# Optimization experiments

Measured on AMD Instinct MI355X. Metric: run time of the kernel, lower is better.

Reference implementation:

```python
import jax, jax.numpy as jnp
import numpy as np

N = 50000          # nodes
E = 800000         # edges
F_IN = 64          # node_features (== LSTM hidden)
C = 100            # conv_out_channels of GatedGraphConv
T = 8              # n_target


def setup_inputs() -> dict:
    key = jax.random.key(0)
    ks = jax.random.split(key, 20)
    s = 0.05
    return {
        "x": jax.random.normal(ks[0], (N, F_IN), jnp.float32),
        "edge_index": jax.random.randint(ks[1], (2, E), 0, N, jnp.int64),
        "edge_weight": jax.random.uniform(ks[2], (E,), jnp.float32),
        "h_0": jax.random.normal(ks[3], (1, N, F_IN), jnp.float32),
        "c_0": jax.random.normal(ks[4], (1, N, F_IN), jnp.float32),
        # GatedGraphConv: weight [num_layers=1, C, C]
        "ggc_w": jax.random.normal(ks[5], (1, C, C), jnp.float32) * s,
        # GRUCell(C, C)
        "gru_w_ih": jax.random.normal(ks[6], (3 * C, C), jnp.float32) * s,
        "gru_w_hh": jax.random.normal(ks[7], (3 * C, C), jnp.float32) * s,
        "gru_b_ih": jnp.zeros((3 * C,), jnp.float32),
        "gru_b_hh": jnp.zeros((3 * C,), jnp.float32),
        # LSTM(input=C, hidden=F_IN, num_layers=1)
        "lstm_w_ih": jax.random.normal(ks[8], (4 * F_IN, C), jnp.float32) * s,
        "lstm_w_hh": jax.random.normal(ks[9], (4 * F_IN, F_IN), jnp.float32) * s,
        "lstm_b_ih": jnp.zeros((4 * F_IN,), jnp.float32),
        "lstm_b_hh": jnp.zeros((4 * F_IN,), jnp.float32),
        # final Linear(F_IN -> T)
        "lin_w": jax.random.normal(ks[10], (T, F_IN), jnp.float32) * s,
        "lin_b": jnp.zeros((T,), jnp.float32),
    }


def reference(x, edge_index, edge_weight, h_0, c_0,
              ggc_w, gru_w_ih, gru_w_hh, gru_b_ih, gru_b_hh,
              lstm_w_ih, lstm_w_hh, lstm_b_ih, lstm_b_hh, lin_w, lin_b):
    src, dst = edge_index[0], edge_index[1]
    # --- GatedGraphConv (1 layer, mean aggr) ---
    xp = jnp.pad(x, ((0, 0), (0, C - x.shape[1])))  # pad features to C
    m = xp @ ggc_w[0]                               # [N, C]
    msg = m[src] * edge_weight[:, None]             # [E, C] gather + weight
    summ = jax.ops.segment_sum(msg, dst, num_segments=N)
    cnt = jax.ops.segment_sum(jnp.ones_like(edge_weight), dst, num_segments=N)
    agg = summ / jnp.maximum(cnt, 1.0)[:, None]     # scatter-mean
    # GRUCell(agg, xp)
    gi = agg @ gru_w_ih.T + gru_b_ih
    gh = xp @ gru_w_hh.T + gru_b_hh
    i_r, i_z, i_n = jnp.split(gi, 3, axis=1)
    h_r, h_z, h_n = jnp.split(gh, 3, axis=1)
    r = jax.nn.sigmoid(i_r + h_r)
    z = jax.nn.sigmoid(i_z + h_z)
    n = jnp.tanh(i_n + r * h_n)
    conv_h = (1.0 - z) * n + z * xp                 # [N, C]
    # --- LSTM, one time step, batch=N, hidden=F_IN ---
    gates = conv_h @ lstm_w_ih.T + lstm_b_ih + h_0[0] @ lstm_w_hh.T + lstm_b_hh
    i_g, f_g, g_g, o_g = jnp.split(gates, 4, axis=1)
    i_g = jax.nn.sigmoid(i_g)
    f_g = jax.nn.sigmoid(f_g)
    g_g = jnp.tanh(g_g)
    o_g = jax.nn.sigmoid(o_g)
    c1 = f_g * c_0[0] + i_g * g_g                   # [N, F_IN]
    h1 = o_g * jnp.tanh(c1)                         # [N, F_IN]
    # --- relu + linear head ---
    out = jax.nn.relu(h1) @ lin_w.T + lin_b         # [N, T]
    return out, h1[None], c1[None]
```

## Files before the change

### kernel.cpp

```cpp
#include <hip/hip_runtime.h>

#define N_NODES 50000
#define N_EDGES 800000
#define F_INF   64
#define C_CH    100
#define T_OUT   8

typedef unsigned short u16;
typedef unsigned int   u32;
typedef __attribute__((ext_vector_type(8))) short bf16x8;
typedef __attribute__((ext_vector_type(4))) float f32x4;

__device__ __forceinline__ float sigmoidf_(float x) {
    return 1.0f / (1.0f + __expf(-x));
}
__device__ __forceinline__ float tanhf_(float x) {
    return 1.0f - 2.0f / (__expf(2.0f * x) + 1.0f);
}
__device__ __forceinline__ u16 f2bf(float f) {
    union { float f; u32 u; } v; v.f = f;
    u32 u = v.u;
    u += 0x7FFF + ((u >> 16) & 1);
    return (u16)(u >> 16);
}
__device__ __forceinline__ float bf2f(u16 h) {
    union { u32 u; float f; } v; v.u = ((u32)h) << 16;
    return v.f;
}
__device__ __forceinline__ float asf_(int i) {
    union { int i; float f; } v; v.i = i; return v.f;
}

#define BK_NPB 64
#define BK_NB  ((N_NODES + BK_NPB - 1) / BK_NPB)
#define BCAP   1280
#define PART_T     1024
#define PART_CHUNK 8192
#define PART_B ((N_EDGES + PART_CHUNK - 1) / PART_CHUNK)
#define PP_XBF_B 391
#define WG2_ELEMS (7 * 4 * 4 * 64 * 8)
#define WL2_ELEMS (4 * 6 * 4 * 64 * 8)
#define PP_W_B ((WG2_ELEMS + WL2_ELEMS) / 1024)
#define PP_B (PART_B + PP_XBF_B + PP_W_B)
#define PP_LDS_SIZE 110880
__global__ __launch_bounds__(PART_T) void k_pp(
    const int* __restrict__ ei, const float* __restrict__ ew,
    const float* __restrict__ x,
    const float* __restrict__ ggc, const float* __restrict__ gwih,
    const float* __restrict__ gwhh,
    const float* __restrict__ lwih, const float* __restrict__ lwhh,
    int* __restrict__ bcur, int2* __restrict__ bucket,
    u16* __restrict__ xbf, u16* __restrict__ Wg2, u16* __restrict__ Wl2) {
    extern __shared__ __align__(16) char pls[];
    int gb = blockIdx.x;
    int tid = threadIdx.x;

    if (gb < PART_B) {
        int2* se    = (int2*)pls;
        int*  gdst  = (int*)(pls + 65536);
        int*  hist  = (int*)(pls + 98304);
        int*  ebase = (int*)(pls + 101432);
        int*  cur   = (int*)(pls + 104560);
        int*  gbase = (int*)(pls + 107688);
        int*  wsum  = (int*)(pls + 110816);
        int e0 = gb * PART_CHUNK;
        int cnt = N_EDGES - e0;
        if (cnt > PART_CHUNK) cnt = PART_CHUNK;

        for (int i = tid; i < BK_NB; i += PART_T) hist[i] = 0;
        __syncthreads();

        int srcr[8], dstr[8]; float wvr[8];
#pragma unroll
        for (int k = 0; k < 8; ++k) {
            int e = tid + k * PART_T;
            if (e < cnt) {
                srcr[k] = ei[e0 + e];
                dstr[k] = ei[N_EDGES + e0 + e];
                wvr[k]  = ew[e0 + e];
                atomicAdd(&hist[dstr[k] >> 6], 1);
            } else dstr[k] = -1;
        }
        __syncthreads();

        {
            int lane = tid & 63, w = tid >> 6;
            int h = (tid < BK_NB) ? hist[tid] : 0;
            int v = h;
#pragma unroll
            for (int off = 1; off < 64; off <<= 1) {
                int u = __shfl_up(v, off, 64);
                if (lane >= off) v += u;
            }
            if (lane == 63) wsum[w] = v;
            __syncthreads();
            if (tid < 16) {
                int s = wsum[tid];
#pragma unroll
                for (int off = 1; off < 16; off <<= 1) {
                    int u = __shfl_up(s, off, 16);
                    if (tid >= off) s += u;
                }
                wsum[tid] = s;
            }
            __syncthreads();
            if (tid < BK_NB) {
                int v2 = v + ((w > 0) ? wsum[w - 1] : 0);
                int ex = v2 - h;
                ebase[tid] = ex;
                cur[tid] = ex;
                gbase[tid] = (h > 0) ? atomicAdd(&bcur[tid * 16], h) : 0;
            }
        }
        __syncthreads();

#pragma unroll
        for (int k = 0; k < 8; ++k) {
            if (dstr[k] >= 0) {
                int b = dstr[k] >> 6;
                int p = atomicAdd(&cur[b], 1);
                int gl = gbase[b] + (p - ebase[b]);
                se[p] = make_int2(srcr[k] | ((dstr[k] & 63) << 16), __float_as_int(wvr[k]));
                gdst[p] = (gl < BCAP) ? (b * BCAP + gl) : -1;
            }
        }
        __syncthreads();

        for (int i = tid; i < cnt; i += PART_T) {
            int g = gdst[i];
            if (g >= 0) bucket[g] = se[i];
        }
        return;
    }

    if (gb < PART_B + PP_XBF_B) {
        int idx = (gb - PART_B) * 1024 + tid;
        if (idx >= N_NODES * F_INF / 8) return;
        float4 a = ((const float4*)x)[idx * 2];
        float4 b = ((const float4*)x)[idx * 2 + 1];
        uint4 p;
        p.x = (u32)f2bf(a.x) | ((u32)f2bf(a.y) << 16);
        p.y = (u32)f2bf(a.z) | ((u32)f2bf(a.w) << 16);
        p.z = (u32)f2bf(b.x) | ((u32)f2bf(b.y) << 16);
        p.w = (u32)f2bf(b.z) | ((u32)f2bf(b.w) << 16);
        ((uint4*)xbf)[idx] = p;
        return;
    }

    int idx = (gb - PART_B - PP_XBF_B) * 1024 + tid;
    if (idx < WG2_ELEMS) {
        int e    = idx & 7;
        int lane = (idx >> 3) & 63;
        int g    = (idx >> 9) & 3;
        int kt   = (idx >> 11) & 3;
        int ct   = idx >> 13;
        int c = ct * 16 + (lane & 15);
        int k = kt * 32 + (lane >> 4) * 8 + e;
        float val = 0.0f;
        if (c < 100) {
            if (g < 3) {
                if (k < 64) {
                    const float* wr = gwih + (g * 100 + c) * 100;
                    const float* gr = ggc + k * 100;
                    float s = 0.0f;
#pragma unroll 4
                    for (int j = 0; j < 100; ++j) s += wr[j] * gr[j];
                    val = s;
                } else if (g < 2) {
                    val = gwhh[(g * 100 + c) * 100 + (k - 64)];
                }
            } else {
                if (k >= 64) val = gwhh[(200 + c) * 100 + (k - 64)];
            }
        }
        Wg2[idx] = f2bf(val);
    } else if (idx < WG2_ELEMS + WL2_ELEMS) {
        int i2 = idx - WG2_ELEMS;
        int e    = i2 & 7;
        int lane = (i2 >> 3) & 63;
        int g    = (i2 >> 9) & 3;
        int ctkt = i2 >> 11;
        int ct = ctkt / 6, kt = ctkt - ct * 6;
        int c = ct * 16 + (lane & 15);
        int k = kt * 32 + (lane >> 4) * 8 + e;
        float val = 0.0f;
        if (k < 100) val = lwih[(g * 64 + c) * 100 + k];
        else if (k >= 128) val = lwhh[(g * 64 + c) * 64 + (k - 128)];
        Wl2[i2] = f2bf(val);
    }
}

__global__ __launch_bounds__(512, 3) void k_bagg(
    const int2* __restrict__ bucket, const int* __restrict__ bcur,
    const u16* __restrict__ xbf, u16* __restrict__ xaggbf) {
    __shared__ int2 se[BCAP];
    __shared__ int  hist[64];
    __shared__ int  base[65];
    __shared__ int  cur[64];
    int tid = threadIdx.x;
    int b = blockIdx.x;
    int n0 = b * BK_NPB;

    if (tid < 64) hist[tid] = 0;
    __syncthreads();

    int cnt = bcur[b * 16];
    if (cnt > BCAP) cnt = BCAP;
    const int2* mybkt = bucket + (size_t)b * BCAP;

    int2 r0 = make_int2(0, 0), r1 = make_int2(0, 0), r2 = make_int2(0, 0);
    int nr = 0;
    if (tid < cnt)        { r0 = mybkt[tid];        atomicAdd(&hist[(r0.x >> 16) & 63], 1); nr = 1; }
    if (tid + 512 < cnt)  { r1 = mybkt[tid + 512];  atomicAdd(&hist[(r1.x >> 16) & 63], 1); nr = 2; }
    if (tid + 1024 < cnt) { r2 = mybkt[tid + 1024]; atomicAdd(&hist[(r2.x >> 16) & 63], 1); nr = 3; }
    __syncthreads();

    if (tid < 64) {
        int h = hist[tid];
        int v = h;
#pragma unroll
        for (int off = 1; off < 64; off <<= 1) {
            int u = __shfl_up(v, off, 64);
            if (tid >= off) v += u;
        }
        base[tid + 1] = v;
        if (tid == 0) base[0] = 0;
        cur[tid] = v - h;
    }
    __syncthreads();

    if (nr > 0) { int p = atomicAdd(&cur[(r0.x >> 16) & 63], 1); se[p] = r0; }
    if (nr > 1) { int p = atomicAdd(&cur[(r1.x >> 16) & 63], 1); se[p] = r1; }
    if (nr > 2) { int p = atomicAdd(&cur[(r2.x >> 16) & 63], 1); se[p] = r2; }
    __syncthreads();

    int w = tid >> 6, lane = tid & 63;
#pragma unroll
    for (int j = 0; j < 8; ++j) {
        int nl = w * 8 + j;
        int s = base[nl], epos = base[nl + 1];
        float acc = 0.0f;
        int i = s;
        for (; i + 3 < epos; i += 4) {
            int2 e0 = se[i], e1 = se[i + 1], e2 = se[i + 2], e3 = se[i + 3];
            float v0 = bf2f(xbf[(size_t)(e0.x & 0xFFFF) * 64 + lane]);
            float v1 = bf2f(xbf[(size_t)(e1.x & 0xFFFF) * 64 + lane]);
            float v2 = bf2f(xbf[(size_t)(e2.x & 0xFFFF) * 64 + lane]);
            float v3 = bf2f(xbf[(size_t)(e3.x & 0xFFFF) * 64 + lane]);
            acc += v0 * asf_(e0.y); acc += v1 * asf_(e1.y);
            acc += v2 * asf_(e2.y); acc += v3 * asf_(e3.y);
        }
        for (; i < epos; ++i) {
            int2 e0 = se[i];
            acc += bf2f(xbf[(size_t)(e0.x & 0xFFFF) * 64 + lane]) * asf_(e0.y);
        }
        int n = n0 + nl;
        if (n < N_NODES) {
            acc /= fmaxf((float)(epos - s), 1.0f);
            xaggbf[(size_t)n * 64 + lane] = f2bf(acc);
        }
    }
}

#define RNN_A2   9728
#define RNN_BIAS 23552
#define RNN_BL   25952
#define RNN_LWF  26976
#define RNN_LBS  29024
__global__ __launch_bounds__(256, 4) void k_rnn(
    const u16* __restrict__ xaggbf, const u16* __restrict__ xbf,
    const float* __restrict__ h0, const float* __restrict__ c0,
    const u16* __restrict__ Wg2, const u16* __restrict__ Wl2,
    const float* __restrict__ gbih, const float* __restrict__ gbhh,
    const float* __restrict__ lbih, const float* __restrict__ lbhh,
    const float* __restrict__ lw, const float* __restrict__ lb,
    float* __restrict__ out, float* __restrict__ h1, float* __restrict__ c1) {
    __shared__ __align__(16) char smem[29056];
    u16*   A1   = (u16*)(smem);
    u16*   A2   = (u16*)(smem + RNN_A2);
    float* bias = (float*)(smem + RNN_BIAS);
    float* bl   = (float*)(smem + RNN_BL);
    float* lwf  = (float*)(smem + RNN_LWF);
    float* lbs  = (float*)(smem + RNN_LBS);
    float* h1s  = (float*)(smem);
    int tid = threadIdx.x;
    int n0 = blockIdx.x * 32;
    int w = tid >> 6, lane = tid & 63, quad = lane >> 4, ln = lane & 15;

    float c0r[2][4];
    {
        int c = w * 16 + ln;
#pragma unroll
        for (int mt = 0; mt < 2; ++mt)
#pragma unroll
            for (int reg = 0; reg < 4; ++reg) {
                int n = n0 + mt * 16 + quad * 4 + reg;
                c0r[mt][reg] = (n < N_NODES) ? c0[(size_t)n * F_INF + c] : 0.0f;
            }
    }
    for (int i = tid; i < 512; i += 256) {
        int row = i >> 4, ch = i & 15;
        int n = n0 + row;
        uint4 v = make_uint4(0, 0, 0, 0);
        if (n < N_NODES)
            v = (ch < 8) ? ((const uint4*)xaggbf)[n * 8 + ch]
                         : ((const uint4*)xbf)[n * 8 + (ch - 8)];
        *(uint4*)(A1 + row * 152 + ch * 8) = v;
    }
    {
        int row = tid >> 3, ch = tid & 7;
        int n = n0 + row;
        uint4 p = make_uint4(0, 0, 0, 0);
        if (n < N_NODES) {
            float4 f0 = ((const float4*)h0)[n * 16 + ch * 2];
            float4 f1 = ((const float4*)h0)[n * 16 + ch * 2 + 1];
            p.x = (u32)f2bf(f0.x) | ((u32)f2bf(f0.y) << 16);
            p.y = (u32)f2bf(f0.z) | ((u32)f2bf(f0.w) << 16);
            p.z = (u32)f2bf(f1.x) | ((u32)f2bf(f1.y) << 16);
            p.w = (u32)f2bf(f1.z) | ((u32)f2bf(f1.w) << 16);
        }
        *(uint4*)(A2 + row * 216 + 128 + ch * 8) = p;
    }
    if (tid < 64) {
        int row = tid >> 1, ch2 = tid & 1;
        *(uint4*)(A2 + row * 216 + 112 + ch2 * 8) = make_uint4(0, 0, 0, 0);
    }
    for (int i = tid; i < 600; i += 256)
        bias[i] = (i < 300) ? gbih[i] : gbhh[i - 300];
    if (tid < 256) bl[tid] = lbih[tid] + lbhh[tid];
    for (int i = tid; i < 512; i += 256) {
        int k = i >> 3, t = i & 7;
        lwf[i] = lw[t * F_INF + k];
    }
    if (tid < 8) lbs[tid] = lb[tid];
    __syncthreads();

    for (int ct = w; ct < 7; ct += 4) {
        int c = ct * 16 + ln;
        float br = 0.f, bz = 0.f, bn2 = 0.f, bh2 = 0.f;
        if (c < 100) {
            br  = bias[c]       + bias[300 + c];
            bz  = bias[100 + c] + bias[400 + c];
            bn2 = bias[200 + c];
            bh2 = bias[500 + c];
        }
        f32x4 ar[2], az[2], an[2], ah[2];
#pragma unroll
        for (int mt = 0; mt < 2; ++mt) {
            ar[mt] = (f32x4){0.f, 0.f, 0.f, 0.f};
            az[mt] = ar[mt]; an[mt] = ar[mt]; ah[mt] = ar[mt];
        }
        const bf16x8* wp = (const bf16x8*)Wg2 + (size_t)(ct * 16) * 64 + lane;
#pragma unroll
        for (int kt = 0; kt < 4; ++kt) {
            bf16x8 b0 = wp[(kt * 4 + 0) * 64];
            bf16x8 b1 = wp[(kt * 4 + 1) * 64];
            bf16x8 b2 = wp[(kt * 4 + 2) * 64];
            bf16x8 b3 = wp[(kt * 4 + 3) * 64];
#pragma unroll
            for (int mt = 0; mt < 2; ++mt) {
                bf16x8 a = *(const bf16x8*)(A1 + (mt * 16 + ln) * 152 + kt * 32 + quad * 8);
                ar[mt] = __builtin_amdgcn_mfma_f32_16x16x32_bf16(a, b0, ar[mt], 0, 0, 0);
                az[mt] = __builtin_amdgcn_mfma_f32_16x16x32_bf16(a, b1, az[mt], 0, 0, 0);
                an[mt] = __builtin_amdgcn_mfma_f32_16x16x32_bf16(a, b2, an[mt], 0, 0, 0);
                ah[mt] = __builtin_amdgcn_mfma_f32_16x16x32_bf16(a, b3, ah[mt], 0, 0, 0);
            }
        }
#pragma unroll
        for (int mt = 0; mt < 2; ++mt) {
#pragma unroll
            for (int reg = 0; reg < 4; ++reg) {
                int m = mt * 16 + quad * 4 + reg;
                float val = 0.0f;
                if (c < 100) {
                    float rv = sigmoidf_(ar[mt][reg] + br);
                    float zv = sigmoidf_(az[mt][reg] + bz);
                    float nv = tanhf_(an[mt][reg] + bn2 + rv * (ah[mt][reg] + bh2));
                    float xp = (c < F_INF) ? bf2f(A1[m * 152 + 64 + c]) : 0.0f;
                    val = (1.0f - zv) * nv + zv * xp;
                }
                A2[m * 216 + c] = f2bf(val);
            }
        }
    }
    __syncthreads();

    float h1v[2][4];
    {
        int ct = w;
        int c = ct * 16 + ln;
        float bi = bl[c], bff = bl[64 + c], bg = bl[128 + c], bo = bl[192 + c];
        f32x4 ai[2], af[2], ag[2], ao[2];
#pragma unroll
        for (int mt = 0; mt < 2; ++mt) {
            ai[mt] = (f32x4){0.f, 0.f, 0.f, 0.f};
            af[mt] = ai[mt]; ag[mt] = ai[mt]; ao[mt] = ai[mt];
        }
        const bf16x8* wp = (const bf16x8*)Wl2 + (size_t)(ct * 24) * 64 + lane;
#pragma unroll
        for (int kt = 0; kt < 6; ++kt) {
            bf16x8 b0 = wp[(kt * 4 + 0) * 64];
            bf16x8 b1 = wp[(kt * 4 + 1) * 64];
            bf16x8 b2 = wp[(kt * 4 + 2) * 64];
            bf16x8 b3 = wp[(kt * 4 + 3) * 64];
#pragma unroll
            for (int mt = 0; mt < 2; ++mt) {
                bf16x8 a = *(const bf16x8*)(A2 + (mt * 16 + ln) * 216 + kt * 32 + quad * 8);
                ai[mt] = __builtin_amdgcn_mfma_f32_16x16x32_bf16(a, b0, ai[mt], 0, 0, 0);
                af[mt] = __builtin_amdgcn_mfma_f32_16x16x32_bf16(a, b1, af[mt], 0, 0, 0);
                ag[mt] = __builtin_amdgcn_mfma_f32_16x16x32_bf16(a, b2, ag[mt], 0, 0, 0);
                ao[mt] = __builtin_amdgcn_mfma_f32_16x16x32_bf16(a, b3, ao[mt], 0, 0, 0);
            }
        }
#pragma unroll
        for (int mt = 0; mt < 2; ++mt) {
#pragma unroll
            for (int reg = 0; reg < 4; ++reg) {
                int m = mt * 16 + quad * 4 + reg;
                int n = n0 + m;
                float iv = sigmoidf_(ai[mt][reg] + bi);
                float fv = sigmoidf_(af[mt][reg] + bff);
                float gv = tanhf_(ag[mt][reg] + bg);
                float ov = sigmoidf_(ao[mt][reg] + bo);
                float cc = fv * c0r[mt][reg] + iv * gv;
                float hh = ov * tanhf_(cc);
                h1v[mt][reg] = hh;
                if (n < N_NODES) {
                    c1[(size_t)n * F_INF + c] = cc;
                    h1[(size_t)n * F_INF + c] = hh;
                }
            }
        }
    }
    __syncthreads();

    {
        int c = w * 16 + ln;
#pragma unroll
        for (int mt = 0; mt < 2; ++mt)
#pragma unroll
            for (int reg = 0; reg < 4; ++reg) {
                int m = mt * 16 + quad * 4 + reg;
                h1s[m * 65 + c] = h1v[mt][reg];
            }
    }
    __syncthreads();

    {
        int nl = tid & 31, t = tid >> 5;
        float acc = lbs[t];
        const float* hr = h1s + nl * 65;
#pragma unroll 8
        for (int k = 0; k < F_INF; ++k)
            acc += fmaxf(hr[k], 0.0f) * lwf[k * 8 + t];
        int n = n0 + nl;
        if (n < N_NODES) out[(size_t)n * T_OUT + t] = acc;
    }
}

extern "C" void kernel_launch(void* const* d_in, const int* in_sizes, int n_in,
                              void* d_out, int out_size, void* d_ws, size_t ws_size,
                              hipStream_t stream) {
    const float* x     = (const float*)d_in[0];
    const int*   ei    = (const int*)d_in[1];
    const float* ew    = (const float*)d_in[2];
    const float* h0    = (const float*)d_in[3];
    const float* c0    = (const float*)d_in[4];
    const float* ggc   = (const float*)d_in[5];
    const float* gwih  = (const float*)d_in[6];
    const float* gwhh  = (const float*)d_in[7];
    const float* gbih  = (const float*)d_in[8];
    const float* gbhh  = (const float*)d_in[9];
    const float* lwih  = (const float*)d_in[10];
    const float* lwhh  = (const float*)d_in[11];
    const float* lbih  = (const float*)d_in[12];
    const float* lbhh  = (const float*)d_in[13];
    const float* lw    = (const float*)d_in[14];
    const float* lb    = (const float*)d_in[15];

    float* out = (float*)d_out;
    float* h1  = out + (size_t)N_NODES * T_OUT;
    float* c1  = h1 + (size_t)N_NODES * F_INF;

    char* ws = (char*)d_ws;
    u16*   xaggbf = (u16*)ws;
    u16*   xbf    = (u16*)(ws + 6400000);
    u16*   Wg2    = (u16*)(ws + 12800000);
    u16*   Wl2    = (u16*)(ws + 12914688);
    int2*  bucket = (int2*)(ws + 13012992);
    int*   bcur   = (int*)(ws + 21020672);

    static int lds_ok = 0;
    if (!lds_ok) {
        hipFuncSetAttribute((const void*)k_pp,
                            hipFuncAttributeMaxDynamicSharedMemorySize, PP_LDS_SIZE);
        lds_ok = 1;
    }

    hipMemsetAsync(bcur, 0, BK_NB * 16 * sizeof(int), stream);

    k_pp<<<PP_B, PART_T, PP_LDS_SIZE, stream>>>(
        ei, ew, x, ggc, gwih, gwhh, lwih, lwhh, bcur, bucket, xbf, Wg2, Wl2);
    k_bagg<<<BK_NB, 512, 0, stream>>>(bucket, bcur, xbf, xaggbf);
    { int b = (N_NODES + 31) / 32;
      k_rnn<<<b, 256, 0, stream>>>(xaggbf, xbf, h0, c0, Wg2, Wl2,
                                   gbih, gbhh, lbih, lbhh, lw, lb,
                                   out, h1, c1); }
}
```

Measured before the change: 189.2 us.

## Fuse bucket aggregation with GRU/LSTM MFMA stage into one kernel

Merges the edge-bucket aggregation kernel and the RNN kernel into a single 512-thread kernel over 64-node buckets, writing the aggregated features straight into LDS as the GRU A-operand instead of round-tripping through a global bf16 buffer. The h0, c0 and x loads are issued before the aggregation so their latency overlaps the gather, and the MFMA work is split across 8 waves covering two 32-row halves. This removes one launch and the xagg global write/read, at the cost of larger LDS use per block and the LDS reuse between the edge list and the A2 tile.

```diff
diff --git a/kernel.cpp b/kernel.cpp
--- a/kernel.cpp
+++ b/kernel.cpp
@@ -190,17 +190,71 @@
     }
 }
 
-__global__ __launch_bounds__(512, 3) void k_bagg(
+#define FU_A1   27648
+#define FU_BIAS 47104
+#define FU_BL   49504
+#define FU_LWF  50528
+#define FU_LBS  52576
+__global__ __launch_bounds__(512, 4) void k_fuse(
     const int2* __restrict__ bucket, const int* __restrict__ bcur,
-    const u16* __restrict__ xbf, u16* __restrict__ xaggbf) {
-    __shared__ int2 se[BCAP];
-    __shared__ int  hist[64];
-    __shared__ int  base[65];
-    __shared__ int  cur[64];
+    const u16* __restrict__ xbf,
+    const float* __restrict__ h0, const float* __restrict__ c0,
+    const u16* __restrict__ Wg2, const u16* __restrict__ Wl2,
+    const float* __restrict__ gbih, const float* __restrict__ gbhh,
+    const float* __restrict__ lbih, const float* __restrict__ lbhh,
+    const float* __restrict__ lw, const float* __restrict__ lb,
+    float* __restrict__ out, float* __restrict__ h1, float* __restrict__ c1) {
+    __shared__ __align__(16) char smem[52608];
+    u16*   A2   = (u16*)(smem);
+    int2*  se   = (int2*)(smem);
+    int*   hist = (int*)(smem + 10240);
+    int*   base = (int*)(smem + 10496);
+    int*   cur  = (int*)(smem + 10760);
+    u16*   A1   = (u16*)(smem + FU_A1);
+    float* bias = (float*)(smem + FU_BIAS);
+    float* bl   = (float*)(smem + FU_BL);
+    float* lwf  = (float*)(smem + FU_LWF);
+    float* lbs  = (float*)(smem + FU_LBS);
+    float* h1s  = (float*)(smem + FU_A1);
     int tid = threadIdx.x;
     int b = blockIdx.x;
     int n0 = b * BK_NPB;
-
+    int w = tid >> 6, lane = tid & 63, quad = lane >> 4, ln = lane & 15;
+
+    float c0r[2][4];
+    {
+        int c = (w >> 1) * 16 + ln;
+#pragma unroll
+        for (int mt = 0; mt < 2; ++mt)
+#pragma unroll
+            for (int reg = 0; reg < 4; ++reg) {
+                int n = n0 + (w & 1) * 32 + mt * 16 + quad * 4 + reg;
+                c0r[mt][reg] = (n < N_NODES) ? c0[(size_t)n * F_INF + c] : 0.0f;
+            }
+    }
+    float4 h0r[2];
+#pragma unroll
+    for (int p = 0; p < 2; ++p) {
+        int i = tid + p * 512;
+        int n = n0 + (i >> 4);
+        h0r[p] = (n < N_NODES) ? ((const float4*)h0)[(size_t)n * 16 + (i & 15)]
+                               : make_float4(0.f, 0.f, 0.f, 0.f);
+    }
+    {
+        int row = tid >> 3, ch = tid & 7;
+        int n = n0 + row;
+        uint4 v = make_uint4(0, 0, 0, 0);
+        if (n < N_NODES) v = ((const uint4*)xbf)[(size_t)n * 8 + ch];
+        *(uint4*)(A1 + row * 152 + 64 + ch * 8) = v;
+    }
+    for (int i = tid; i < 600; i += 512)
+        bias[i] = (i < 300) ? gbih[i] : gbhh[i - 300];
+    if (tid < 256) bl[tid] = lbih[tid] + lbhh[tid];
+    if (tid < 512) {
+        int k = tid >> 3, t = tid & 7;
+        lwf[tid] = lw[t * F_INF + k];
+    }
+    if (tid < 8) lbs[tid] = lb[tid];
     if (tid < 64) hist[tid] = 0;
     __syncthreads();
 
@@ -234,7 +288,6 @@
     if (nr > 2) { int p = atomicAdd(&cur[(r2.x >> 16) & 63], 1); se[p] = r2; }
     __syncthreads();
 
-    int w = tid >> 6, lane = tid & 63;
 #pragma unroll
     for (int j = 0; j < 8; ++j) {
         int nl = w * 8 + j;
@@ -254,88 +307,26 @@
             int2 e0 = se[i];
             acc += bf2f(xbf[(size_t)(e0.x & 0xFFFF) * 64 + lane]) * asf_(e0.y);
         }
-        int n = n0 + nl;
-        if (n < N_NODES) {
-            acc /= fmaxf((float)(epos - s), 1.0f);
-            xaggbf[(size_t)n * 64 + lane] = f2bf(acc);
-        }
-    }
-}
-
-#define RNN_A2   9728
-#define RNN_BIAS 23552
-#define RNN_BL   25952
-#define RNN_LWF  26976
-#define RNN_LBS  29024
-__global__ __launch_bounds__(256, 4) void k_rnn(
-    const u16* __restrict__ xaggbf, const u16* __restrict__ xbf,
-    const float* __restrict__ h0, const float* __restrict__ c0,
-    const u16* __restrict__ Wg2, const u16* __restrict__ Wl2,
-    const float* __restrict__ gbih, const float* __restrict__ gbhh,
-    const float* __restrict__ lbih, const float* __restrict__ lbhh,
-    const float* __restrict__ lw, const float* __restrict__ lb,
-    float* __restrict__ out, float* __restrict__ h1, float* __restrict__ c1) {
-    __shared__ __align__(16) char smem[29056];
-    u16*   A1   = (u16*)(smem);
-    u16*   A2   = (u16*)(smem + RNN_A2);
-    float* bias = (float*)(smem + RNN_BIAS);
-    float* bl   = (float*)(smem + RNN_BL);
-    float* lwf  = (float*)(smem + RNN_LWF);
-    float* lbs  = (float*)(smem + RNN_LBS);
-    float* h1s  = (float*)(smem);
-    int tid = threadIdx.x;
-    int n0 = blockIdx.x * 32;
-    int w = tid >> 6, lane = tid & 63, quad = lane >> 4, ln = lane & 15;
-
-    float c0r[2][4];
-    {
-        int c = w * 16 + ln;
-#pragma unroll
-        for (int mt = 0; mt < 2; ++mt)
-#pragma unroll
-            for (int reg = 0; reg < 4; ++reg) {
-                int n = n0 + mt * 16 + quad * 4 + reg;
-                c0r[mt][reg] = (n < N_NODES) ? c0[(size_t)n * F_INF + c] : 0.0f;
-            }
-    }
-    for (int i = tid; i < 512; i += 256) {
-        int row = i >> 4, ch = i & 15;
-        int n = n0 + row;
-        uint4 v = make_uint4(0, 0, 0, 0);
-        if (n < N_NODES)
-            v = (ch < 8) ? ((const uint4*)xaggbf)[n * 8 + ch]
-                         : ((const uint4*)xbf)[n * 8 + (ch - 8)];
-        *(uint4*)(A1 + row * 152 + ch * 8) = v;
-    }
-    {
-        int row = tid >> 3, ch = tid & 7;
-        int n = n0 + row;
-        uint4 p = make_uint4(0, 0, 0, 0);
-        if (n < N_NODES) {
-            float4 f0 = ((const float4*)h0)[n * 16 + ch * 2];
-            float4 f1 = ((const float4*)h0)[n * 16 + ch * 2 + 1];
-            p.x = (u32)f2bf(f0.x) | ((u32)f2bf(f0.y) << 16);
-            p.y = (u32)f2bf(f0.z) | ((u32)f2bf(f0.w) << 16);
-            p.z = (u32)f2bf(f1.x) | ((u32)f2bf(f1.y) << 16);
-            p.w = (u32)f2bf(f1.z) | ((u32)f2bf(f1.w) << 16);
-        }
-        *(uint4*)(A2 + row * 216 + 128 + ch * 8) = p;
-    }
-    if (tid < 64) {
+        acc /= fmaxf((float)(epos - s), 1.0f);
+        A1[nl * 152 + lane] = f2bf(acc);
+    }
+    __syncthreads();
+
+#pragma unroll
+    for (int p = 0; p < 2; ++p) {
+        int i = tid + p * 512;
+        int node = i >> 4, ch = i & 15;
+        u32 lo = (u32)f2bf(h0r[p].x) | ((u32)f2bf(h0r[p].y) << 16);
+        u32 hi = (u32)f2bf(h0r[p].z) | ((u32)f2bf(h0r[p].w) << 16);
+        *(uint2*)(A2 + node * 216 + 128 + ch * 4) = make_uint2(lo, hi);
+    }
+    if (tid < 128) {
         int row = tid >> 1, ch2 = tid & 1;
         *(uint4*)(A2 + row * 216 + 112 + ch2 * 8) = make_uint4(0, 0, 0, 0);
     }
-    for (int i = tid; i < 600; i += 256)
-        bias[i] = (i < 300) ? gbih[i] : gbhh[i - 300];
-    if (tid < 256) bl[tid] = lbih[tid] + lbhh[tid];
-    for (int i = tid; i < 512; i += 256) {
-        int k = i >> 3, t = i & 7;
-        lwf[i] = lw[t * F_INF + k];
-    }
-    if (tid < 8) lbs[tid] = lb[tid];
-    __syncthreads();
-
-    for (int ct = w; ct < 7; ct += 4) {
+
+    for (int id = w; id < 14; id += 8) {
+        int ct = id % 7, mh = id / 7;
         int c = ct * 16 + ln;
         float br = 0.f, bz = 0.f, bn2 = 0.f, bh2 = 0.f;
         if (c < 100) {
@@ -359,7 +350,7 @@
             bf16x8 b3 = wp[(kt * 4 + 3) * 64];
 #pragma unroll
             for (int mt = 0; mt < 2; ++mt) {
-                bf16x8 a = *(const bf16x8*)(A1 + (mt * 16 + ln) * 152 + kt * 32 + quad * 8);
+                bf16x8 a = *(const bf16x8*)(A1 + (mh * 32 + mt * 16 + ln) * 152 + kt * 32 + quad * 8);
                 ar[mt] = __builtin_amdgcn_mfma_f32_16x16x32_bf16(a, b0, ar[mt], 0, 0, 0);
                 az[mt] = __builtin_amdgcn_mfma_f32_16x16x32_bf16(a, b1, az[mt], 0, 0, 0);
                 an[mt] = __builtin_amdgcn_mfma_f32_16x16x32_bf16(a, b2, an[mt], 0, 0, 0);
@@ -370,7 +361,7 @@
         for (int mt = 0; mt < 2; ++mt) {
 #pragma unroll
             for (int reg = 0; reg < 4; ++reg) {
-                int m = mt * 16 + quad * 4 + reg;
+                int m = mh * 32 + mt * 16 + quad * 4 + reg;
                 float val = 0.0f;
                 if (c < 100) {
                     float rv = sigmoidf_(ar[mt][reg] + br);
@@ -387,7 +378,7 @@
 
     float h1v[2][4];
     {
-        int ct = w;
+        int ct = w >> 1, mg = w & 1;
         int c = ct * 16 + ln;
         float bi = bl[c], bff = bl[64 + c], bg = bl[128 + c], bo = bl[192 + c];
         f32x4 ai[2], af[2], ag[2], ao[2];
@@ -405,7 +396,7 @@
             bf16x8 b3 = wp[(kt * 4 + 3) * 64];
 #pragma unroll
             for (int mt = 0; mt < 2; ++mt) {
-                bf16x8 a = *(const bf16x8*)(A2 + (mt * 16 + ln) * 216 + kt * 32 + quad * 8);
+                bf16x8 a = *(const bf16x8*)(A2 + (mg * 32 + mt * 16 + ln) * 216 + kt * 32 + quad * 8);
                 ai[mt] = __builtin_amdgcn_mfma_f32_16x16x32_bf16(a, b0, ai[mt], 0, 0, 0);
                 af[mt] = __builtin_amdgcn_mfma_f32_16x16x32_bf16(a, b1, af[mt], 0, 0, 0);
                 ag[mt] = __builtin_amdgcn_mfma_f32_16x16x32_bf16(a, b2, ag[mt], 0, 0, 0);
@@ -416,7 +407,7 @@
         for (int mt = 0; mt < 2; ++mt) {
 #pragma unroll
             for (int reg = 0; reg < 4; ++reg) {
-                int m = mt * 16 + quad * 4 + reg;
+                int m = mg * 32 + mt * 16 + quad * 4 + reg;
                 int n = n0 + m;
                 float iv = sigmoidf_(ai[mt][reg] + bi);
                 float fv = sigmoidf_(af[mt][reg] + bff);
@@ -435,19 +426,19 @@
     __syncthreads();
 
     {
-        int c = w * 16 + ln;
+        int c = (w >> 1) * 16 + ln;
 #pragma unroll
         for (int mt = 0; mt < 2; ++mt)
 #pragma unroll
             for (int reg = 0; reg < 4; ++reg) {
-                int m = mt * 16 + quad * 4 + reg;
+                int m = (w & 1) * 32 + mt * 16 + quad * 4 + reg;
                 h1s[m * 65 + c] = h1v[mt][reg];
             }
     }
     __syncthreads();
 
     {
-        int nl = tid & 31, t = tid >> 5;
+        int nl = tid & 63, t = tid >> 6;
         float acc = lbs[t];
         const float* hr = h1s + nl * 65;
 #pragma unroll 8
@@ -483,12 +474,11 @@
     float* c1  = h1 + (size_t)N_NODES * F_INF;
 
     char* ws = (char*)d_ws;
-    u16*   xaggbf = (u16*)ws;
-    u16*   xbf    = (u16*)(ws + 6400000);
-    u16*   Wg2    = (u16*)(ws + 12800000);
-    u16*   Wl2    = (u16*)(ws + 12914688);
-    int2*  bucket = (int2*)(ws + 13012992);
-    int*   bcur   = (int*)(ws + 21020672);
+    u16*   xbf    = (u16*)ws;
+    u16*   Wg2    = (u16*)(ws + 6400000);
+    u16*   Wl2    = (u16*)(ws + 6514688);
+    int2*  bucket = (int2*)(ws + 6612992);
+    int*   bcur   = (int*)(ws + 14620672);
 
     static int lds_ok = 0;
     if (!lds_ok) {
@@ -501,9 +491,7 @@
 
     k_pp<<<PP_B, PART_T, PP_LDS_SIZE, stream>>>(
         ei, ew, x, ggc, gwih, gwhh, lwih, lwhh, bcur, bucket, xbf, Wg2, Wl2);
-    k_bagg<<<BK_NB, 512, 0, stream>>>(bucket, bcur, xbf, xaggbf);
-    { int b = (N_NODES + 31) / 32;
-      k_rnn<<<b, 256, 0, stream>>>(xaggbf, xbf, h0, c0, Wg2, Wl2,
-                                   gbih, gbhh, lbih, lbhh, lw, lb,
-                                   out, h1, c1); }
-}
+    k_fuse<<<BK_NB, 512, 0, stream>>>(bucket, bcur, xbf, h0, c0, Wg2, Wl2,
+                                      gbih, gbhh, lbih, lbhh, lw, lb,
+                                      out, h1, c1);
+}
```

Result: slower. 204.4 us (+8.1%).

## Give each wave its own 16-node tile in RNN kernel to drop block barriers

Applied to the files above, without the earlier changes.

The RNN kernel is restructured so each wavefront owns a private 16-row tile of nodes with its own LDS staging, looping over all GRU and LSTM column tiles itself. Blocks now cover 64 nodes, and the intermediate __syncthreads between GRU, LSTM and the linear head are removed, leaving only the initial barrier for shared biases. In exchange, each wave reloads every weight fragment from global memory for only one M-tile, which halves weight reuse per load. LDS per block nearly doubles, and the occupancy hint is lowered from 4 to 3 blocks.

```diff
diff --git a/kernel.cpp b/kernel.cpp
--- a/kernel.cpp
+++ b/kernel.cpp
@@ -262,12 +262,11 @@
     }
 }
 
-#define RNN_A2   9728
-#define RNN_BIAS 23552
-#define RNN_BL   25952
-#define RNN_LWF  26976
-#define RNN_LBS  29024
-__global__ __launch_bounds__(256, 4) void k_rnn(
+#define RNN_BIAS 47104
+#define RNN_BL   49504
+#define RNN_LWF  50528
+#define RNN_LBS  52576
+__global__ __launch_bounds__(256, 3) void k_rnn(
     const u16* __restrict__ xaggbf, const u16* __restrict__ xbf,
     const float* __restrict__ h0, const float* __restrict__ c0,
     const u16* __restrict__ Wg2, const u16* __restrict__ Wl2,
@@ -275,55 +274,52 @@
     const float* __restrict__ lbih, const float* __restrict__ lbhh,
     const float* __restrict__ lw, const float* __restrict__ lb,
     float* __restrict__ out, float* __restrict__ h1, float* __restrict__ c1) {
-    __shared__ __align__(16) char smem[29056];
-    u16*   A1   = (u16*)(smem);
-    u16*   A2   = (u16*)(smem + RNN_A2);
+    __shared__ __align__(16) char smem[52608];
+    int tid = threadIdx.x;
+    int w = tid >> 6, lane = tid & 63, quad = lane >> 4, ln = lane & 15;
+    u16*   A1   = (u16*)(smem + w * 4864);
+    u16*   A2   = (u16*)(smem + 19456 + w * 6912);
     float* bias = (float*)(smem + RNN_BIAS);
     float* bl   = (float*)(smem + RNN_BL);
     float* lwf  = (float*)(smem + RNN_LWF);
     float* lbs  = (float*)(smem + RNN_LBS);
-    float* h1s  = (float*)(smem);
-    int tid = threadIdx.x;
-    int n0 = blockIdx.x * 32;
-    int w = tid >> 6, lane = tid & 63, quad = lane >> 4, ln = lane & 15;
-
-    float c0r[2][4];
-    {
-        int c = w * 16 + ln;
-#pragma unroll
-        for (int mt = 0; mt < 2; ++mt)
-#pragma unroll
-            for (int reg = 0; reg < 4; ++reg) {
-                int n = n0 + mt * 16 + quad * 4 + reg;
-                c0r[mt][reg] = (n < N_NODES) ? c0[(size_t)n * F_INF + c] : 0.0f;
-            }
-    }
-    for (int i = tid; i < 512; i += 256) {
+    float* h1s  = (float*)(smem + w * 4864);
+    int n0 = blockIdx.x * 64 + w * 16;
+
+    float c0r[4][4];
+#pragma unroll
+    for (int ct = 0; ct < 4; ++ct)
+#pragma unroll
+        for (int reg = 0; reg < 4; ++reg) {
+            int n = n0 + quad * 4 + reg;
+            c0r[ct][reg] = (n < N_NODES) ? c0[(size_t)n * F_INF + ct * 16 + ln] : 0.0f;
+        }
+
+#pragma unroll
+    for (int r = 0; r < 4; ++r) {
+        int i = lane + r * 64;
         int row = i >> 4, ch = i & 15;
         int n = n0 + row;
         uint4 v = make_uint4(0, 0, 0, 0);
         if (n < N_NODES)
-            v = (ch < 8) ? ((const uint4*)xaggbf)[n * 8 + ch]
-                         : ((const uint4*)xbf)[n * 8 + (ch - 8)];
+            v = (ch < 8) ? ((const uint4*)xaggbf)[(size_t)n * 8 + ch]
+                         : ((const uint4*)xbf)[(size_t)n * 8 + (ch - 8)];
         *(uint4*)(A1 + row * 152 + ch * 8) = v;
     }
+#pragma unroll
+    for (int r = 0; r < 4; ++r) {
+        int i = lane + r * 64;
+        int row = i >> 4, ch = i & 15;
+        int n = n0 + row;
+        float4 f = make_float4(0.f, 0.f, 0.f, 0.f);
+        if (n < N_NODES) f = ((const float4*)h0)[(size_t)n * 16 + ch];
+        u32 lo = (u32)f2bf(f.x) | ((u32)f2bf(f.y) << 16);
+        u32 hi = (u32)f2bf(f.z) | ((u32)f2bf(f.w) << 16);
+        *(uint2*)(A2 + row * 216 + 128 + ch * 4) = make_uint2(lo, hi);
+    }
     {
-        int row = tid >> 3, ch = tid & 7;
-        int n = n0 + row;
-        uint4 p = make_uint4(0, 0, 0, 0);
-        if (n < N_NODES) {
-            float4 f0 = ((const float4*)h0)[n * 16 + ch * 2];
-            float4 f1 = ((const float4*)h0)[n * 16 + ch * 2 + 1];
-            p.x = (u32)f2bf(f0.x) | ((u32)f2bf(f0.y) << 16);
-            p.y = (u32)f2bf(f0.z) | ((u32)f2bf(f0.w) << 16);
-            p.z = (u32)f2bf(f1.x) | ((u32)f2bf(f1.y) << 16);
-            p.w = (u32)f2bf(f1.z) | ((u32)f2bf(f1.w) << 16);
-        }
-        *(uint4*)(A2 + row * 216 + 128 + ch * 8) = p;
-    }
-    if (tid < 64) {
-        int row = tid >> 1, ch2 = tid & 1;
-        *(uint4*)(A2 + row * 216 + 112 + ch2 * 8) = make_uint4(0, 0, 0, 0);
+        int row = lane & 15, q = lane >> 4;
+        if (q < 2) *(uint4*)(A2 + row * 216 + 112 + q * 8) = make_uint4(0, 0, 0, 0);
     }
     for (int i = tid; i < 600; i += 256)
         bias[i] = (i < 300) ? gbih[i] : gbhh[i - 300];
@@ -335,7 +331,8 @@
     if (tid < 8) lbs[tid] = lb[tid];
     __syncthreads();
 
-    for (int ct = w; ct < 7; ct += 4) {
+#pragma unroll 1
+    for (int ct = 0; ct < 7; ++ct) {
         int c = ct * 16 + ln;
         float br = 0.f, bz = 0.f, bn2 = 0.f, bh2 = 0.f;
         if (c < 100) {
@@ -344,12 +341,8 @@
             bn2 = bias[200 + c];
             bh2 = bias[500 + c];
         }
-        f32x4 ar[2], az[2], an[2], ah[2];
-#pragma unroll
-        for (int mt = 0; mt < 2; ++mt) {
-            ar[mt] = (f32x4){0.f, 0.f, 0.f, 0.f};
-            az[mt] = ar[mt]; an[mt] = ar[mt]; ah[mt] = ar[mt];
-        }
+        f32x4 ar = (f32x4){0.f, 0.f, 0.f, 0.f};
+        f32x4 az = ar, an = ar, ah = ar;
         const bf16x8* wp = (const bf16x8*)Wg2 + (size_t)(ct * 16) * 64 + lane;
 #pragma unroll
         for (int kt = 0; kt < 4; ++kt) {
@@ -357,45 +350,33 @@
             bf16x8 b1 = wp[(kt * 4 + 1) * 64];
             bf16x8 b2 = wp[(kt * 4 + 2) * 64];
             bf16x8 b3 = wp[(kt * 4 + 3) * 64];
-#pragma unroll
-            for (int mt = 0; mt < 2; ++mt) {
-                bf16x8 a = *(const bf16x8*)(A1 + (mt * 16 + ln) * 152 + kt * 32 + quad * 8);
-                ar[mt] = __builtin_amdgcn_mfma_f32_16x16x32_bf16(a, b0, ar[mt], 0, 0, 0);
-                az[mt] = __builtin_amdgcn_mfma_f32_16x16x32_bf16(a, b1, az[mt], 0, 0, 0);
-                an[mt] = __builtin_amdgcn_mfma_f32_16x16x32_bf16(a, b2, an[mt], 0, 0, 0);
-                ah[mt] = __builtin_amdgcn_mfma_f32_16x16x32_bf16(a, b3, ah[mt], 0, 0, 0);
-            }
-        }
-#pragma unroll
-        for (int mt = 0; mt < 2; ++mt) {
-#pragma unroll
-            for (int reg = 0; reg < 4; ++reg) {
-                int m = mt * 16 + quad * 4 + reg;
-                float val = 0.0f;
-                if (c < 100) {
-                    float rv = sigmoidf_(ar[mt][reg] + br);
-                    float zv = sigmoidf_(az[mt][reg] + bz);
-                    float nv = tanhf_(an[mt][reg] + bn2 + rv * (ah[mt][reg] + bh2));
-                    float xp = (c < F_INF) ? bf2f(A1[m * 152 + 64 + c]) : 0.0f;
-                    val = (1.0f - zv) * nv + zv * xp;
-                }
-                A2[m * 216 + c] = f2bf(val);
-            }
-        }
-    }
-    __syncthreads();
-
-    float h1v[2][4];
-    {
-        int ct = w;
+            bf16x8 a = *(const bf16x8*)(A1 + ln * 152 + kt * 32 + quad * 8);
+            ar = __builtin_amdgcn_mfma_f32_16x16x32_bf16(a, b0, ar, 0, 0, 0);
+            az = __builtin_amdgcn_mfma_f32_16x16x32_bf16(a, b1, az, 0, 0, 0);
+            an = __builtin_amdgcn_mfma_f32_16x16x32_bf16(a, b2, an, 0, 0, 0);
+            ah = __builtin_amdgcn_mfma_f32_16x16x32_bf16(a, b3, ah, 0, 0, 0);
+        }
+#pragma unroll
+        for (int reg = 0; reg < 4; ++reg) {
+            int m = quad * 4 + reg;
+            float val = 0.0f;
+            if (c < 100) {
+                float rv = sigmoidf_(ar[reg] + br);
+                float zv = sigmoidf_(az[reg] + bz);
+                float nv = tanhf_(an[reg] + bn2 + rv * (ah[reg] + bh2));
+                float xp = (c < F_INF) ? bf2f(A1[m * 152 + 64 + c]) : 0.0f;
+                val = (1.0f - zv) * nv + zv * xp;
+            }
+            A2[m * 216 + c] = f2bf(val);
+        }
+    }
+
+#pragma unroll 1
+    for (int ct = 0; ct < 4; ++ct) {
         int c = ct * 16 + ln;
         float bi = bl[c], bff = bl[64 + c], bg = bl[128 + c], bo = bl[192 + c];
-        f32x4 ai[2], af[2], ag[2], ao[2];
-#pragma unroll
-        for (int mt = 0; mt < 2; ++mt) {
-            ai[mt] = (f32x4){0.f, 0.f, 0.f, 0.f};
-            af[mt] = ai[mt]; ag[mt] = ai[mt]; ao[mt] = ai[mt];
-        }
+        f32x4 ai = (f32x4){0.f, 0.f, 0.f, 0.f};
+        f32x4 af = ai, ag = ai, ao = ai;
         const bf16x8* wp = (const bf16x8*)Wl2 + (size_t)(ct * 24) * 64 + lane;
 #pragma unroll
         for (int kt = 0; kt < 6; ++kt) {
@@ -403,58 +384,43 @@
             bf16x8 b1 = wp[(kt * 4 + 1) * 64];
             bf16x8 b2 = wp[(kt * 4 + 2) * 64];
             bf16x8 b3 = wp[(kt * 4 + 3) * 64];
-#pragma unroll
-            for (int mt = 0; mt < 2; ++mt) {
-                bf16x8 a = *(const bf16x8*)(A2 + (mt * 16 + ln) * 216 + kt * 32 + quad * 8);
-                ai[mt] = __builtin_amdgcn_mfma_f32_16x16x32_bf16(a, b0, ai[mt], 0, 0, 0);
-                af[mt] = __builtin_amdgcn_mfma_f32_16x16x32_bf16(a, b1, af[mt], 0, 0, 0);
-                ag[mt] = __builtin_amdgcn_mfma_f32_16x16x32_bf16(a, b2, ag[mt], 0, 0, 0);
-                ao[mt] = __builtin_amdgcn_mfma_f32_16x16x32_bf16(a, b3, ao[mt], 0, 0, 0);
-            }
-        }
-#pragma unroll
-        for (int mt = 0; mt < 2; ++mt) {
-#pragma unroll
-            for (int reg = 0; reg < 4; ++reg) {
-                int m = mt * 16 + quad * 4 + reg;
-                int n = n0 + m;
-                float iv = sigmoidf_(ai[mt][reg] + bi);
-                float fv = sigmoidf_(af[mt][reg] + bff);
-                float gv = tanhf_(ag[mt][reg] + bg);
-                float ov = sigmoidf_(ao[mt][reg] + bo);
-                float cc = fv * c0r[mt][reg] + iv * gv;
-                float hh = ov * tanhf_(cc);
-                h1v[mt][reg] = hh;
-                if (n < N_NODES) {
-                    c1[(size_t)n * F_INF + c] = cc;
-                    h1[(size_t)n * F_INF + c] = hh;
-                }
-            }
-        }
-    }
-    __syncthreads();
+            bf16x8 a = *(const bf16x8*)(A2 + ln * 216 + kt * 32 + quad * 8);
+            ai = __builtin_amdgcn_mfma_f32_16x16x32_bf16(a, b0, ai, 0, 0, 0);
+            af = __builtin_amdgcn_mfma_f32_16x16x32_bf16(a, b1, af, 0, 0, 0);
+            ag = __builtin_amdgcn_mfma_f32_16x16x32_bf16(a, b2, ag, 0, 0, 0);
+            ao = __builtin_amdgcn_mfma_f32_16x16x32_bf16(a, b3, ao, 0, 0, 0);
+        }
+#pragma unroll
+        for (int reg = 0; reg < 4; ++reg) {
+            int m = quad * 4 + reg;
+            int n = n0 + m;
+            float iv = sigmoidf_(ai[reg] + bi);
+            float fv = sigmoidf_(af[reg] + bff);
+            float gv = tanhf_(ag[reg] + bg);
+            float ov = sigmoidf_(ao[reg] + bo);
+            float cc = fv * c0r[ct][reg] + iv * gv;
+            float hh = ov * tanhf_(cc);
+            h1s[m * 65 + c] = hh;
+            if (n < N_NODES) {
+                c1[(size_t)n * F_INF + c] = cc;
+                h1[(size_t)n * F_INF + c] = hh;
+            }
+        }
+    }
 
     {
-        int c = w * 16 + ln;
-#pragma unroll
-        for (int mt = 0; mt < 2; ++mt)
-#pragma unroll
-            for (int reg = 0; reg < 4; ++reg) {
-                int m = mt * 16 + quad * 4 + reg;
-                h1s[m * 65 + c] = h1v[mt][reg];
-            }
-    }
-    __syncthreads();
-
-    {
-        int nl = tid & 31, t = tid >> 5;
-        float acc = lbs[t];
-        const float* hr = h1s + nl * 65;
+        int t = lane & 7, nl0 = lane >> 3;
+#pragma unroll
+        for (int r2 = 0; r2 < 2; ++r2) {
+            int nl = nl0 + r2 * 8;
+            float acc = lbs[t];
+            const float* hr = h1s + nl * 65;
 #pragma unroll 8
-        for (int k = 0; k < F_INF; ++k)
-            acc += fmaxf(hr[k], 0.0f) * lwf[k * 8 + t];
-        int n = n0 + nl;
-        if (n < N_NODES) out[(size_t)n * T_OUT + t] = acc;
+            for (int k = 0; k < F_INF; ++k)
+                acc += fmaxf(hr[k], 0.0f) * lwf[k * 8 + t];
+            int n = n0 + nl;
+            if (n < N_NODES) out[(size_t)n * T_OUT + t] = acc;
+        }
     }
 }
 
@@ -502,7 +468,7 @@
     k_pp<<<PP_B, PART_T, PP_LDS_SIZE, stream>>>(
         ei, ew, x, ggc, gwih, gwhh, lwih, lwhh, bcur, bucket, xbf, Wg2, Wl2);
     k_bagg<<<BK_NB, 512, 0, stream>>>(bucket, bcur, xbf, xaggbf);
-    { int b = (N_NODES + 31) / 32;
+    { int b = (N_NODES + 63) / 64;
       k_rnn<<<b, 256, 0, stream>>>(xaggbf, xbf, h0, c0, Wg2, Wl2,
                                    gbih, gbhh, lbih, lbhh, lw, lb,
                                    out, h1, c1); }
```

After: 213.8 us. 13.0% more time.
